# Performance work log

Measured on AMD Instinct MI355X. Metric: run time of the kernel, lower is better.

## Reference

```python
import jax, jax.numpy as jnp
import numpy as np

N, G, S = 51200, 512, 100   # nodes, graphs, nodes per graph
E = 512000                   # edges (within-graph)
F, H, D = 64, 4, 64
HD = H * D                   # 256
C = 10
RATIO = 0.8
NEG = -1e30


def _seg_softmax(logits, seg, mask, num_seg):
    # masked softmax over edges grouped by destination node
    lg = jnp.where(mask[:, None], logits, NEG)
    m = jax.lax.stop_gradient(jax.ops.segment_max(lg, seg, num_segments=num_seg))
    ex = jnp.where(mask[:, None], jnp.exp(lg - m[seg]), 0.0)
    s = jax.ops.segment_sum(ex, seg, num_segments=num_seg)
    return ex / jnp.maximum(s[seg], 1e-16)


def _gat_conv(x, src, dst, nmask, emask, W, att, b, Wres):
    # PyG GATConv: heads=4, concat=True, add_self_loops=True, residual Linear
    h = (x @ W).reshape(N, H, D)
    a_src = (h * att[0]).sum(-1)   # [N,H]
    a_dst = (h * att[1]).sum(-1)
    loop = jnp.arange(N, dtype=src.dtype)
    s2 = jnp.concatenate([src, loop])
    d2 = jnp.concatenate([dst, loop])
    em2 = jnp.concatenate([emask, nmask])
    logits = jax.nn.leaky_relu(a_src[s2] + a_dst[d2], 0.2)   # [E+N,H]
    alpha = _seg_softmax(logits, d2, em2, N)
    out = jax.ops.segment_sum(h[s2] * alpha[:, :, None], d2, num_segments=N)
    out = out.reshape(N, HD) + x @ Wres + b
    return out * nmask[:, None]


def _gt_conv(x, src, dst, nmask, emask, Wqkv, bqkv, Wskip, bskip):
    # PyG TransformerConv: heads=4, concat=True, root_weight=True (lin_skip)
    qkv = (x @ Wqkv + bqkv).reshape(N, 3, H, D)
    q, k, v = qkv[:, 0], qkv[:, 1], qkv[:, 2]
    logits = (q[dst] * k[src]).sum(-1) * (1.0 / np.sqrt(D))   # [E,H]
    alpha = _seg_softmax(logits, dst, emask, N)
    out = jax.ops.segment_sum(v[src] * alpha[:, :, None], dst, num_segments=N)
    return (out.reshape(N, HD) + x @ Wskip + bskip) * nmask[:, None]


def _topk_pool(x, w, batch, nmask, emask, src, dst):
    # PyG TopKPooling: score=tanh(x.w/|w|), keep top ceil(0.8*n) per graph,
    # x <- x*score, drop edges touching removed nodes. Masked (static-shape) form.
    score = jnp.tanh((x @ w) / jnp.linalg.norm(w))
    keyv = jnp.where(nmask, score, NEG)
    # composite key: sort by graph id, then by score descending (dead nodes last)
    ck = batch.astype(jnp.float32) * 4.0 - jnp.clip(keyv, -1.5, 1.5)
    order = jnp.argsort(ck)
    n_alive = jax.ops.segment_sum(nmask.astype(jnp.int32), batch, num_segments=G)
    k = jnp.ceil(RATIO * n_alive.astype(jnp.float32)).astype(jnp.int32)
    counts = jax.ops.segment_sum(jnp.ones(N, jnp.int32), batch, num_segments=G)
    start = jnp.cumsum(counts) - counts
    gs = batch[order]
    rank = jnp.arange(N, dtype=jnp.int32) - start[gs]
    keep = jnp.zeros(N, bool).at[order].set(rank < k[gs]) & nmask
    x_new = jnp.where(keep[:, None], x * score[:, None], 0.0)
    emask_new = emask & keep[src] & keep[dst]
    return x_new, keep, emask_new


def _readout(x, batch, nmask):
    # torch_geometric gmp || gap over alive nodes
    mx = jax.ops.segment_max(jnp.where(nmask[:, None], x, NEG), batch, num_segments=G)
    sm = jax.ops.segment_sum(x * nmask[:, None].astype(x.dtype), batch, num_segments=G)
    cnt = jax.ops.segment_sum(nmask.astype(x.dtype), batch, num_segments=G)
    return jnp.concatenate([mx, sm / jnp.maximum(cnt, 1.0)[:, None]], axis=1)


def _branch(x, src, dst, batch, conv, layers, pool_w):
    nmask = jnp.ones(N, bool)
    emask = jnp.ones(E, bool)
    acc = jnp.zeros((G, 2 * HD), x.dtype)
    for i in range(3):
        x = jax.nn.relu(conv(x, src, dst, nmask, emask, *layers[i]))
        x, nmask, emask = _topk_pool(x, pool_w[i], batch, nmask, emask, src, dst)
        acc = acc + _readout(x, batch, nmask)
    return acc


def _forward(x, edge_index, batch, gat1_W, gat1_att, gat1_b, gat1_res, gat2_W, gat2_att, gat2_b, gat2_res, gat3_W, gat3_att, gat3_b, gat3_res, gat_pool_w, gt1_Wqkv, gt1_bqkv, gt1_Wskip, gt1_bskip, gt2_Wqkv, gt2_bqkv, gt2_Wskip, gt2_bskip, gt3_Wqkv, gt3_bqkv, gt3_Wskip, gt3_bskip, gt_pool_w, lin1_W, lin1_b, lin2_W, lin2_b, lin3_W, lin3_b):
    src, dst = edge_index[0], edge_index[1]
    gat_layers = [(gat1_W, gat1_att, gat1_b, gat1_res),
                  (gat2_W, gat2_att, gat2_b, gat2_res),
                  (gat3_W, gat3_att, gat3_b, gat3_res)]
    gt_layers = [(gt1_Wqkv, gt1_bqkv, gt1_Wskip, gt1_bskip),
                 (gt2_Wqkv, gt2_bqkv, gt2_Wskip, gt2_bskip),
                 (gt3_Wqkv, gt3_bqkv, gt3_Wskip, gt3_bskip)]
    h1 = _branch(x, src, dst, batch, _gat_conv, gat_layers, gat_pool_w)
    h2 = _branch(x, src, dst, batch, _gt_conv, gt_layers, gt_pool_w)
    h = jnp.concatenate([h1, h2], axis=1)   # [G, 1024]
    h = jax.nn.relu(h @ lin1_W + lin1_b)
    # dropout p=0.5 skipped (eval mode)
    h = jax.nn.relu(h @ lin2_W + lin2_b)
    return jax.nn.log_softmax(h @ lin3_W + lin3_b, axis=-1)


def setup_inputs():
    keys = iter(jax.random.split(jax.random.key(0), 64))
    def nrm(shape, scale):
        return jax.random.normal(next(keys), shape, jnp.float32) * scale
    inp = {}
    inp["x"] = nrm((N, F), 1.0)
    src = jax.random.randint(next(keys), (E,), 0, N, jnp.int32)
    off = jax.random.randint(next(keys), (E,), 0, S, jnp.int32)
    dst = (src // S) * S + off   # keep edges within the source node's graph
    inp["edge_index"] = jnp.stack([src, dst])
    inp["batch"] = jnp.arange(N, dtype=jnp.int32) // S
    ins = [F, HD, HD]
    for i in range(3):
        fi = ins[i]
        sc = 1.0 / np.sqrt(fi)
        inp[f"gat{i+1}_W"] = nrm((fi, HD), sc)
        inp[f"gat{i+1}_att"] = nrm((2, H, D), 0.1)
        inp[f"gat{i+1}_b"] = jnp.zeros((HD,), jnp.float32)
        inp[f"gat{i+1}_res"] = nrm((fi, HD), sc)
        inp[f"gt{i+1}_Wqkv"] = nrm((fi, 3 * HD), sc)
        inp[f"gt{i+1}_bqkv"] = jnp.zeros((3 * HD,), jnp.float32)
        inp[f"gt{i+1}_Wskip"] = nrm((fi, HD), sc)
        inp[f"gt{i+1}_bskip"] = jnp.zeros((HD,), jnp.float32)
    inp["gat_pool_w"] = nrm((3, HD), 0.1)
    inp["gt_pool_w"] = nrm((3, HD), 0.1)
    inp["lin1_W"] = nrm((4 * HD, 128), 1.0 / np.sqrt(4 * HD))
    inp["lin1_b"] = jnp.zeros((128,), jnp.float32)
    inp["lin2_W"] = nrm((128, 64), 1.0 / np.sqrt(128.0))
    inp["lin2_b"] = jnp.zeros((64,), jnp.float32)
    inp["lin3_W"] = nrm((64, C), 1.0 / np.sqrt(64.0))
    inp["lin3_b"] = jnp.zeros((C,), jnp.float32)
    return inp


def reference(x, edge_index, batch, gat1_W, gat1_att, gat1_b, gat1_res, gat2_W, gat2_att, gat2_b, gat2_res, gat3_W, gat3_att, gat3_b, gat3_res, gat_pool_w, gt1_Wqkv, gt1_bqkv, gt1_Wskip, gt1_bskip, gt2_Wqkv, gt2_bqkv, gt2_Wskip, gt2_bskip, gt3_Wqkv, gt3_bqkv, gt3_Wskip, gt3_bskip, gt_pool_w, lin1_W, lin1_b, lin2_W, lin2_b, lin3_W, lin3_b):
    return _forward(x, edge_index, batch, gat1_W, gat1_att, gat1_b, gat1_res, gat2_W, gat2_att, gat2_b, gat2_res, gat3_W, gat3_att, gat3_b, gat3_res, gat_pool_w, gt1_Wqkv, gt1_bqkv, gt1_Wskip, gt1_bskip, gt2_Wqkv, gt2_bqkv, gt2_Wskip, gt2_bskip, gt3_Wqkv, gt3_bqkv, gt3_Wskip, gt3_bskip, gt_pool_w, lin1_W, lin1_b, lin2_W, lin2_b, lin3_W, lin3_b)
```

## Files before the change

### kernel.cpp

```cpp
#include <hip/hip_runtime.h>
#include <hip/hip_bf16.h>
#include <math.h>

#define N_NODES 51200
#define N_GRAPHS 512
#define S_NODES 100
#define N_EDGES 512000
#define HDF 256
#define NEGF (-1e30f)
#define DCAP 128

typedef short bf16x8 __attribute__((ext_vector_type(8)));
typedef float f32x4 __attribute__((ext_vector_type(4)));

__device__ inline unsigned short f2b(float x) {
    union { float f; unsigned u; } v; v.f = x;
    unsigned r = v.u + 0x7FFFu + ((v.u >> 16) & 1u);
    return (unsigned short)(r >> 16);
}
__device__ inline float b2f(unsigned short b) {
    union { float f; unsigned u; } v; v.u = ((unsigned)b) << 16; return v.f;
}

__global__ void set_int(int* __restrict__ p, int v, int n) {
    int i = blockIdx.x * 256 + threadIdx.x;
    if (i < n) p[i] = v;
}

__global__ void init_zero(int* __restrict__ deg, int* __restrict__ cursor,
                          float* __restrict__ acc1, float* __restrict__ acc2) {
    int i = blockIdx.x * 256 + threadIdx.x;
    if (i < N_NODES) { deg[i] = 0; cursor[i] = 0; }
    acc1[i] = 0.f;
    acc2[i] = 0.f;
}

struct WSplitDesc { const float* W; unsigned short* Wh; unsigned short* Wl; int K, NC; };
struct WSplitPack { WSplitDesc d[12]; };
__global__ void wsplit_all(WSplitPack p) {
    WSplitDesc d = p.d[blockIdx.y];
    int idx = blockIdx.x * 256 + threadIdx.x;
    if (idx >= d.K * d.NC) return;
    int k = idx / d.NC, c = idx - k * d.NC;
    float v = d.W[idx];
    unsigned short h = f2b(v);
    int o = ((k >> 3) * d.NC + c) * 8 + (k & 7);
    d.Wh[o] = h;
    d.Wl[o] = f2b(v - b2f(h));
}

__global__ __launch_bounds__(512) void mfma_gemm(
    const float* __restrict__ A,
    const unsigned short* __restrict__ Bh_g, const unsigned short* __restrict__ Bl_g,
    const float* __restrict__ bias, float* __restrict__ C,
    int K, int NC,
    const float* __restrict__ agg, int aggStride,
    const int* __restrict__ nmaskArr,
    const float* __restrict__ rowScale, const int* __restrict__ rsMask)
{
    __shared__ unsigned short Ah[4 * 128 * 8];
    __shared__ unsigned short Al[4 * 128 * 8];
    int row0 = blockIdx.y * 128, col0 = blockIdx.x * 256;
    int t = threadIdx.x;
    int lane = t & 63, w = t >> 6;
    int wr = w >> 2, wc = w & 3;
    int l15 = lane & 15, l4 = lane >> 4;
    f32x4 acc[4][4];
    #pragma unroll
    for (int m = 0; m < 4; ++m)
        #pragma unroll
        for (int n = 0; n < 4; ++n) acc[m][n] = (f32x4){0.f, 0.f, 0.f, 0.f};

    int arow = t & 127, akg = t >> 7;
    float ascale = 1.f;
    if (rowScale) ascale = rsMask[row0 + arow] ? rowScale[row0 + arow] : 0.f;

    for (int k0 = 0; k0 < K; k0 += 32) {
        const float* ap = A + (size_t)(row0 + arow) * K + k0 + akg * 8;
        float4 a0 = *(const float4*)ap;
        float4 a1 = *(const float4*)(ap + 4);
        float av[8] = {a0.x, a0.y, a0.z, a0.w, a1.x, a1.y, a1.z, a1.w};
        int abase = (akg * 128 + arow) * 8;
        #pragma unroll
        for (int j = 0; j < 8; ++j) {
            float s = av[j] * ascale;
            unsigned short h = f2b(s);
            Ah[abase + j] = h;
            Al[abase + j] = f2b(s - b2f(h));
        }
        __syncthreads();
        bf16x8 bh[4], bl[4];
        size_t brow = (size_t)((k0 >> 3) + l4) * NC;
        #pragma unroll
        for (int n = 0; n < 4; ++n) {
            size_t gb = (brow + col0 + wc * 64 + n * 16 + l15) * 8;
            bh[n] = *(const bf16x8*)&Bh_g[gb];
            bl[n] = *(const bf16x8*)&Bl_g[gb];
        }
        #pragma unroll
        for (int m = 0; m < 4; ++m) {
            int idx = (l4 * 128 + wr * 64 + m * 16 + l15) * 8;
            bf16x8 ah = *(bf16x8*)&Ah[idx];
            bf16x8 al = *(bf16x8*)&Al[idx];
            #pragma unroll
            for (int n = 0; n < 4; ++n) {
                acc[m][n] = __builtin_amdgcn_mfma_f32_16x16x32_bf16(ah, bh[n], acc[m][n], 0, 0, 0);
                acc[m][n] = __builtin_amdgcn_mfma_f32_16x16x32_bf16(ah, bl[n], acc[m][n], 0, 0, 0);
                acc[m][n] = __builtin_amdgcn_mfma_f32_16x16x32_bf16(al, bh[n], acc[m][n], 0, 0, 0);
            }
        }
        __syncthreads();
    }
    bool fused = (agg != nullptr);
    #pragma unroll
    for (int m = 0; m < 4; ++m) {
        #pragma unroll
        for (int n = 0; n < 4; ++n) {
            int col = col0 + wc * 64 + n * 16 + l15;
            float bv = bias ? bias[col] : 0.f;
            #pragma unroll
            for (int r = 0; r < 4; ++r) {
                int row = row0 + wr * 64 + m * 16 + l4 * 4 + r;
                float v = acc[m][n][r] + bv;
                if (fused) {
                    v += agg[(size_t)row * aggStride + col];
                    float nm = nmaskArr[row] ? 1.f : 0.f;
                    C[(size_t)row * 256 + col] = fmaxf(v, 0.f) * nm;
                } else {
                    C[(size_t)row * NC + col] = v;
                }
            }
        }
    }
}

__global__ void count_deg(const int* __restrict__ dst, int* __restrict__ deg) {
    int e = blockIdx.x * 256 + threadIdx.x;
    atomicAdd(&deg[dst[e]], 1);
}

__global__ __launch_bounds__(1024) void scan_deg(const int* __restrict__ deg,
                                                 int* __restrict__ rowStart) {
    __shared__ int part[1024];
    int t = threadIdx.x;
    const int chunk = N_NODES / 1024;
    int s = t * chunk;
    int sum = 0;
    for (int i = 0; i < chunk; ++i) sum += deg[s + i];
    part[t] = sum;
    __syncthreads();
    for (int d = 1; d < 1024; d <<= 1) {
        int v = (t >= d) ? part[t - d] : 0;
        __syncthreads();
        part[t] += v;
        __syncthreads();
    }
    int excl = (t == 0) ? 0 : part[t - 1];
    for (int i = 0; i < chunk; ++i) { rowStart[s + i] = excl; excl += deg[s + i]; }
    if (t == 1023) rowStart[N_NODES] = part[1023];
}

__global__ void scatter_edges(const int* __restrict__ src, const int* __restrict__ dst,
                              int* __restrict__ cursor, const int* __restrict__ rowStart,
                              int* __restrict__ csrSrc) {
    int e = blockIdx.x * 256 + threadIdx.x;
    int d = dst[e];
    int p = atomicAdd(&cursor[d], 1);
    csrSrc[rowStart[d] + p] = src[e];
}

__global__ __launch_bounds__(256) void gat_att_pw(const float* __restrict__ hfeat,
                                                  const float* __restrict__ att,
                                                  float* __restrict__ aS,
                                                  float* __restrict__ aD) {
    int t = threadIdx.x, w = t >> 6, l = t & 63;
    int i = blockIdx.x * 4 + w;
    int h = l >> 4, g16 = l & 15;
    float4 hv = *(const float4*)&hfeat[i * HDF + l * 4];
    float4 a0 = *(const float4*)&att[l * 4];
    float4 a1 = *(const float4*)&att[256 + l * 4];
    float p0 = hv.x * a0.x + hv.y * a0.y + hv.z * a0.z + hv.w * a0.w;
    float p1 = hv.x * a1.x + hv.y * a1.y + hv.z * a1.z + hv.w * a1.w;
    p0 += __shfl_xor(p0, 1, 64);  p1 += __shfl_xor(p1, 1, 64);
    p0 += __shfl_xor(p0, 2, 64);  p1 += __shfl_xor(p1, 2, 64);
    p0 += __shfl_xor(p0, 4, 64);  p1 += __shfl_xor(p1, 4, 64);
    p0 += __shfl_xor(p0, 8, 64);  p1 += __shfl_xor(p1, 8, 64);
    if (g16 == 0) { aS[i * 4 + h] = p0; aD[i * 4 + h] = p1; }
}

__global__ __launch_bounds__(256) void gat_edge_pg(
    const float* __restrict__ hfeat, const float* __restrict__ aS, const float* __restrict__ aD,
    const int* __restrict__ rowStart, const int* __restrict__ csrSrc,
    const int* __restrict__ nmask,
    float* __restrict__ aggOut)
{
    int bid = blockIdx.x;
    int t = threadIdx.x, w = t >> 6, l = t & 63;
    int i = (bid & 7) * (N_NODES / 8) + (bid >> 3) * 4 + w;
    int h = l >> 4, g16 = l & 15;
    __shared__ float sL[4][4][DCAP + 8];
    __shared__ int   sS[4][DCAP + 8];
    if (!nmask[i]) {
        *(float4*)&aggOut[i * HDF + l * 4] = make_float4(0.f, 0.f, 0.f, 0.f);
        return;
    }
    int rs = rowStart[i];
    int deg = min(rowStart[i + 1] - rs, DCAP);
    float adh = aD[i * 4 + h];
    for (int j = 0; j < deg; ++j) {
        int s_ = csrSrc[rs + j];
        int ok = nmask[s_];
        float lg = aS[s_ * 4 + h] + adh;
        lg = (lg >= 0.f) ? lg : 0.2f * lg;
        if (g16 == 0) sL[w][h][j] = ok ? lg : NEGF;
        if (l == 0) sS[w][j] = ok ? s_ : -1;
    }
    {
        float lg = aS[i * 4 + h] + adh;
        lg = (lg >= 0.f) ? lg : 0.2f * lg;
        if (g16 == 0) sL[w][h][deg] = lg;
        if (l == 0) sS[w][deg] = i;
    }
    int tot = deg + 1;
    float m = NEGF;
    for (int j = g16; j < tot; j += 16) m = fmaxf(m, sL[w][h][j]);
    m = fmaxf(m, __shfl_xor(m, 1, 64));
    m = fmaxf(m, __shfl_xor(m, 2, 64));
    m = fmaxf(m, __shfl_xor(m, 4, 64));
    m = fmaxf(m, __shfl_xor(m, 8, 64));
    float sum = 0.f;
    for (int j = g16; j < tot; j += 16) {
        float lv = sL[w][h][j];
        float e = (lv > -1e29f) ? __expf(lv - m) : 0.f;
        sL[w][h][j] = e;
        sum += e;
    }
    sum += __shfl_xor(sum, 1, 64);
    sum += __shfl_xor(sum, 2, 64);
    sum += __shfl_xor(sum, 4, 64);
    sum += __shfl_xor(sum, 8, 64);
    float inv = 1.f / fmaxf(sum, 1e-16f);
    float4 a4 = make_float4(0.f, 0.f, 0.f, 0.f);
    for (int j = 0; j < tot; ++j) {
        int s_ = sS[w][j];
        if (s_ < 0) continue;
        float a = sL[w][h][j] * inv;
        float4 v4 = *(const float4*)&hfeat[s_ * HDF + l * 4];
        a4.x += a * v4.x; a4.y += a * v4.y; a4.z += a * v4.z; a4.w += a * v4.w;
    }
    *(float4*)&aggOut[i * HDF + l * 4] = a4;
}

__global__ __launch_bounds__(256) void gt_edge_pg(
    float* __restrict__ qkv,
    const int* __restrict__ rowStart, const int* __restrict__ csrSrc,
    const int* __restrict__ nmask)
{
    int bid = blockIdx.x;
    int t = threadIdx.x, w = t >> 6, l = t & 63;
    int i = (bid & 7) * (N_NODES / 8) + (bid >> 3) * 4 + w;
    int h = l >> 4, g16 = l & 15;
    __shared__ float sL[4][4][DCAP + 8];
    __shared__ int   sS[4][DCAP + 8];
    if (!nmask[i]) {
        *(float4*)&qkv[i * 768 + l * 4] = make_float4(0.f, 0.f, 0.f, 0.f);
        return;
    }
    int rs = rowStart[i];
    int deg = min(rowStart[i + 1] - rs, DCAP);
    float4 q4 = *(const float4*)&qkv[i * 768 + l * 4];
    for (int j = 0; j < deg; ++j) {
        int s_ = csrSrc[rs + j];
        int ok = nmask[s_];
        float4 k4 = *(const float4*)&qkv[s_ * 768 + 256 + l * 4];
        float p = q4.x * k4.x + q4.y * k4.y + q4.z * k4.z + q4.w * k4.w;
        p += __shfl_xor(p, 1, 64);
        p += __shfl_xor(p, 2, 64);
        p += __shfl_xor(p, 4, 64);
        p += __shfl_xor(p, 8, 64);
        if (g16 == 0) sL[w][h][j] = ok ? p * 0.125f : NEGF;
        if (l == 0) sS[w][j] = ok ? s_ : -1;
    }
    float m = NEGF;
    for (int j = g16; j < deg; j += 16) m = fmaxf(m, sL[w][h][j]);
    m = fmaxf(m, __shfl_xor(m, 1, 64));
    m = fmaxf(m, __shfl_xor(m, 2, 64));
    m = fmaxf(m, __shfl_xor(m, 4, 64));
    m = fmaxf(m, __shfl_xor(m, 8, 64));
    float sum = 0.f;
    for (int j = g16; j < deg; j += 16) {
        float lv = sL[w][h][j];
        float e = (lv > -1e29f) ? __expf(lv - m) : 0.f;
        sL[w][h][j] = e;
        sum += e;
    }
    sum += __shfl_xor(sum, 1, 64);
    sum += __shfl_xor(sum, 2, 64);
    sum += __shfl_xor(sum, 4, 64);
    sum += __shfl_xor(sum, 8, 64);
    float inv = 1.f / fmaxf(sum, 1e-16f);
    float4 a4 = make_float4(0.f, 0.f, 0.f, 0.f);
    for (int j = 0; j < deg; ++j) {
        int s_ = sS[w][j];
        if (s_ < 0) continue;
        float a = sL[w][h][j] * inv;
        float4 v4 = *(const float4*)&qkv[s_ * 768 + 512 + l * 4];
        a4.x += a * v4.x; a4.y += a * v4.y; a4.z += a * v4.z; a4.w += a * v4.w;
    }
    *(float4*)&qkv[i * 768 + l * 4] = a4;
}

__global__ __launch_bounds__(256) void spr_kernel(
    const float* __restrict__ x, const float* __restrict__ w,
    float* __restrict__ score, int* __restrict__ nmask, float* __restrict__ acc)
{
    int g = blockIdx.x, t = threadIdx.x;
    int wv = t >> 6, l = t & 63;
    __shared__ float sW[256];
    __shared__ float sRaw[104];
    __shared__ float sFin[104];
    __shared__ int   sKeep[104];
    __shared__ float swn;
    __shared__ int cnt_s;
    if (t == 0) cnt_s = 0;
    sW[t] = w[t];
    __syncthreads();
    if (wv == 0) {
        float dw = 0.f;
        #pragma unroll
        for (int c = 0; c < 4; ++c) { float v = sW[l + c * 64]; dw += v * v; }
        #pragma unroll
        for (int o = 32; o > 0; o >>= 1) dw += __shfl_down(dw, o, 64);
        if (l == 0) swn = sqrtf(dw);
    }
    int base = g * S_NODES;
    for (int u = 0; u < 25; ++u) {
        int nl = wv * 25 + u;
        float dx = 0.f;
        #pragma unroll
        for (int c = 0; c < 4; ++c) {
            int cc = l + c * 64;
            dx += x[(size_t)(base + nl) * HDF + cc] * sW[cc];
        }
        #pragma unroll
        for (int o = 32; o > 0; o >>= 1) dx += __shfl_down(dx, o, 64);
        if (l == 0) sRaw[nl] = dx;
    }
    __syncthreads();
    int alive = 0;
    float ck = -2.0f;
    if (t < S_NODES) {
        float sc = tanhf(sRaw[t] / swn);
        sFin[t] = sc;
        score[base + t] = sc;
        alive = nmask[base + t];
        ck = alive ? sc : -1.5f;
        sRaw[t] = ck;
        if (alive) atomicAdd(&cnt_s, 1);
    }
    __syncthreads();
    int k = (int)ceilf(0.8f * (float)cnt_s);
    if (t < S_NODES) {
        int rank = 0;
        for (int jj = 0; jj < S_NODES; ++jj) {
            float o = sRaw[jj];
            rank += (o > ck || (o == ck && jj < t)) ? 1 : 0;
        }
        int kp = (alive && rank < k) ? 1 : 0;
        sKeep[t] = kp;
        nmask[base + t] = kp;
    }
    __syncthreads();
    float mx = NEGF, sm = 0.f, cnt = 0.f;
    for (int o = 0; o < S_NODES; o += 4) {
        float v0 = x[(size_t)(base + o + 0) * HDF + t];
        float v1 = x[(size_t)(base + o + 1) * HDF + t];
        float v2 = x[(size_t)(base + o + 2) * HDF + t];
        float v3 = x[(size_t)(base + o + 3) * HDF + t];
        if (sKeep[o + 0]) { float v = v0 * sFin[o + 0]; mx = fmaxf(mx, v); sm += v; cnt += 1.f; }
        if (sKeep[o + 1]) { float v = v1 * sFin[o + 1]; mx = fmaxf(mx, v); sm += v; cnt += 1.f; }
        if (sKeep[o + 2]) { float v = v2 * sFin[o + 2]; mx = fmaxf(mx, v); sm += v; cnt += 1.f; }
        if (sKeep[o + 3]) { float v = v3 * sFin[o + 3]; mx = fmaxf(mx, v); sm += v; cnt += 1.f; }
    }
    acc[(size_t)g * 512 + t] += mx;
    acc[(size_t)g * 512 + 256 + t] += sm / fmaxf(cnt, 1.f);
}

__global__ __launch_bounds__(128) void mlp_kernel(
    const float* __restrict__ acc1, const float* __restrict__ acc2,
    const float* __restrict__ W1, const float* __restrict__ b1,
    const float* __restrict__ W2, const float* __restrict__ b2,
    const float* __restrict__ W3, const float* __restrict__ b3,
    float* __restrict__ out)
{
    int g = blockIdx.x, t = threadIdx.x;
    __shared__ float hrow[1024];
    __shared__ float h1s[128];
    __shared__ float h2s[64];
    __shared__ float o3[10];
    for (int j = t; j < 512; j += 128) {
        hrow[j] = acc1[(size_t)g * 512 + j];
        hrow[512 + j] = acc2[(size_t)g * 512 + j];
    }
    __syncthreads();
    float s = b1[t];
    for (int kx = 0; kx < 1024; ++kx) s += hrow[kx] * W1[(size_t)kx * 128 + t];
    h1s[t] = fmaxf(s, 0.f);
    __syncthreads();
    if (t < 64) {
        float s2 = b2[t];
        for (int kx = 0; kx < 128; ++kx) s2 += h1s[kx] * W2[kx * 64 + t];
        h2s[t] = fmaxf(s2, 0.f);
    }
    __syncthreads();
    if (t < 10) {
        float s3 = b3[t];
        for (int kx = 0; kx < 64; ++kx) s3 += h2s[kx] * W3[kx * 10 + t];
        o3[t] = s3;
    }
    __syncthreads();
    if (t < 10) {
        float m = o3[0];
        for (int j = 1; j < 10; ++j) m = fmaxf(m, o3[j]);
        float se = 0.f;
        for (int j = 0; j < 10; ++j) se += expf(o3[j] - m);
        out[g * 10 + t] = o3[t] - m - logf(se);
    }
}

extern "C" void kernel_launch(void* const* d_in, const int* in_sizes, int n_in,
                              void* d_out, int out_size, void* d_ws, size_t ws_size,
                              hipStream_t stream) {
    (void)n_in; (void)out_size; (void)ws_size;
    const float* x0 = (const float*)d_in[0];
    const int* src = (const int*)d_in[1];
    const int* dst = src + N_EDGES;

    bool dictOrder = (in_sizes[7] == 64 * 768);
    const float *gatW[3], *gatAtt[3], *gatB[3], *gatRes[3];
    const float *gtWqkv[3], *gtBqkv[3], *gtWskip[3], *gtBskip[3];
    const float *gatPool, *gtPool;
    if (dictOrder) {
        for (int l = 0; l < 3; ++l) {
            int b = 3 + l * 8;
            gatW[l]    = (const float*)d_in[b + 0];
            gatAtt[l]  = (const float*)d_in[b + 1];
            gatB[l]    = (const float*)d_in[b + 2];
            gatRes[l]  = (const float*)d_in[b + 3];
            gtWqkv[l]  = (const float*)d_in[b + 4];
            gtBqkv[l]  = (const float*)d_in[b + 5];
            gtWskip[l] = (const float*)d_in[b + 6];
            gtBskip[l] = (const float*)d_in[b + 7];
        }
        gatPool = (const float*)d_in[27];
        gtPool  = (const float*)d_in[28];
    } else {
        for (int l = 0; l < 3; ++l) {
            int b = 3 + l * 4;
            gatW[l]   = (const float*)d_in[b + 0];
            gatAtt[l] = (const float*)d_in[b + 1];
            gatB[l]   = (const float*)d_in[b + 2];
            gatRes[l] = (const float*)d_in[b + 3];
            int c = 16 + l * 4;
            gtWqkv[l]  = (const float*)d_in[c + 0];
            gtBqkv[l]  = (const float*)d_in[c + 1];
            gtWskip[l] = (const float*)d_in[c + 2];
            gtBskip[l] = (const float*)d_in[c + 3];
        }
        gatPool = (const float*)d_in[15];
        gtPool  = (const float*)d_in[28];
    }
    const float* lin1W = (const float*)d_in[29];
    const float* lin1b = (const float*)d_in[30];
    const float* lin2W = (const float*)d_in[31];
    const float* lin2b = (const float*)d_in[32];
    const float* lin3W = (const float*)d_in[33];
    const float* lin3b = (const float*)d_in[34];

    char* wsp = (char*)d_ws;
    size_t off = 0;
    auto carve = [&](size_t bytes) -> void* {
        void* p = wsp + off;
        off += (bytes + 255) & ~(size_t)255;
        return p;
    };
    float* bufX   = (float*)carve((size_t)N_NODES * HDF * 4);
    float* bufH   = (float*)carve((size_t)N_NODES * 768 * 4);
    float* aS     = (float*)carve((size_t)N_NODES * 4 * 4);
    float* aD     = (float*)carve((size_t)N_NODES * 4 * 4);
    float* scoreB = (float*)carve((size_t)N_NODES * 4);
    int* nmask    = (int*)carve((size_t)N_NODES * 4);
    int* deg      = (int*)carve((size_t)N_NODES * 4);
    int* rowStart = (int*)carve((size_t)(N_NODES + 1) * 4);
    int* cursor   = (int*)carve((size_t)N_NODES * 4);
    int* csrSrc   = (int*)carve((size_t)N_EDGES * 4);
    float* acc1   = (float*)carve((size_t)N_GRAPHS * 512 * 4);
    float* acc2   = (float*)carve((size_t)N_GRAPHS * 512 * 4);
    const int wElems = 884736;
    unsigned short* whBase = (unsigned short*)carve((size_t)wElems * 2);
    unsigned short* wlBase = (unsigned short*)carve((size_t)wElems * 2);
    float* ysec   = bufH + (size_t)N_NODES * HDF;

    unsigned short *WH[12], *WL[12];
    {
        WSplitPack pack;
        int o = 0, maxSz = 0;
        for (int l = 0; l < 3; ++l) {
            int fi = (l == 0) ? 64 : 256;
            int sz[4] = {fi * 256, fi * 256, fi * 768, fi * 256};
            const float* Wp[4] = {gatW[l], gatRes[l], gtWqkv[l], gtWskip[l]};
            int NCs[4] = {256, 256, 768, 256};
            for (int q = 0; q < 4; ++q) {
                int idx = l * 4 + q;
                WH[idx] = whBase + o;
                WL[idx] = wlBase + o;
                pack.d[idx] = {Wp[q], WH[idx], WL[idx], fi, NCs[q]};
                if (sz[q] > maxSz) maxSz = sz[q];
                o += sz[q];
            }
        }
        wsplit_all<<<dim3((maxSz + 255) / 256, 12), 256, 0, stream>>>(pack);
    }

    init_zero<<<(N_GRAPHS * 512) / 256, 256, 0, stream>>>(deg, cursor, acc1, acc2);
    count_deg<<<N_EDGES / 256, 256, 0, stream>>>(dst, deg);
    scan_deg<<<1, 1024, 0, stream>>>(deg, rowStart);
    scatter_edges<<<N_EDGES / 256, 256, 0, stream>>>(src, dst, cursor, rowStart, csrSrc);

    for (int br = 0; br < 2; ++br) {
        bool isGAT = (br == 0);
        float* acc = isGAT ? acc1 : acc2;
        const float* poolW = isGAT ? gatPool : gtPool;
        set_int<<<N_NODES / 256, 256, 0, stream>>>(nmask, 1, N_NODES);
        const float* xcur = x0;
        int fi = 64;
        for (int l = 0; l < 3; ++l) {
            const float* rs = (l == 0) ? nullptr : scoreB;
            const int* rsm = (l == 0) ? nullptr : nmask;
            if (isGAT) {
                mfma_gemm<<<dim3(1, N_NODES / 128), 512, 0, stream>>>(
                    xcur, WH[l * 4 + 0], WL[l * 4 + 0], nullptr, bufH, fi, 256,
                    nullptr, 0, nullptr, rs, rsm);
                gat_att_pw<<<N_NODES / 4, 256, 0, stream>>>(bufH, gatAtt[l], aS, aD);
                gat_edge_pg<<<N_NODES / 4, 256, 0, stream>>>(bufH, aS, aD, rowStart,
                                                             csrSrc, nmask, ysec);
                mfma_gemm<<<dim3(1, N_NODES / 128), 512, 0, stream>>>(
                    xcur, WH[l * 4 + 1], WL[l * 4 + 1], gatB[l], bufX, fi, 256,
                    ysec, HDF, nmask, rs, rsm);
            } else {
                mfma_gemm<<<dim3(3, N_NODES / 128), 512, 0, stream>>>(
                    xcur, WH[l * 4 + 2], WL[l * 4 + 2], gtBqkv[l], bufH, fi, 768,
                    nullptr, 0, nullptr, rs, rsm);
                gt_edge_pg<<<N_NODES / 4, 256, 0, stream>>>(bufH, rowStart, csrSrc,
                                                            nmask);
                mfma_gemm<<<dim3(1, N_NODES / 128), 512, 0, stream>>>(
                    xcur, WH[l * 4 + 3], WL[l * 4 + 3], gtBskip[l], bufX, fi, 256,
                    bufH , 768, nmask, rs, rsm);
            }
            spr_kernel<<<N_GRAPHS, 256, 0, stream>>>(bufX, poolW + l * HDF,
                                                     scoreB, nmask, acc);
            xcur = bufX;
            fi = HDF;
        }
    }
    mlp_kernel<<<N_GRAPHS, 128, 0, stream>>>(acc1, acc2, lin1W, lin1b, lin2W, lin2b,
                                             lin3W, lin3b, (float*)d_out);
}
```

Baseline: 1.329 ms.

## Double-buffer GEMM A tiles and parallelize edge neighbor preload in GAT/GT kernels

The MFMA GEMM now uses two LDS buffers for the A tile. It prefetches the next K-slice from global memory while the current slice is consumed, which drops one barrier per iteration. The GAT and GT edge kernels load neighbor indices and masks in parallel across the wavefront into shared memory, replacing a serial per-edge loop. GAT logits are also computed in parallel across the 16 lanes per head, and GT skips K loads for masked neighbors. The cost is double the LDS use in the GEMM, which may lower occupancy.

```diff
diff --git a/kernel.cpp b/kernel.cpp
--- a/kernel.cpp
+++ b/kernel.cpp
@@ -58,8 +58,8 @@
     const int* __restrict__ nmaskArr,
     const float* __restrict__ rowScale, const int* __restrict__ rsMask)
 {
-    __shared__ unsigned short Ah[4 * 128 * 8];
-    __shared__ unsigned short Al[4 * 128 * 8];
+    __shared__ unsigned short Ah[2][4 * 128 * 8];
+    __shared__ unsigned short Al[2][4 * 128 * 8];
     int row0 = blockIdx.y * 128, col0 = blockIdx.x * 256;
     int t = threadIdx.x;
     int lane = t & 63, w = t >> 6;
@@ -74,21 +74,31 @@
     int arow = t & 127, akg = t >> 7;
     float ascale = 1.f;
     if (rowScale) ascale = rsMask[row0 + arow] ? rowScale[row0 + arow] : 0.f;
-
-    for (int k0 = 0; k0 < K; k0 += 32) {
-        const float* ap = A + (size_t)(row0 + arow) * K + k0 + akg * 8;
-        float4 a0 = *(const float4*)ap;
-        float4 a1 = *(const float4*)(ap + 4);
+    const float* aptr = A + (size_t)(row0 + arow) * K + akg * 8;
+    int abase = (akg * 128 + arow) * 8;
+
+    {
+        float4 a0 = *(const float4*)aptr;
+        float4 a1 = *(const float4*)(aptr + 4);
         float av[8] = {a0.x, a0.y, a0.z, a0.w, a1.x, a1.y, a1.z, a1.w};
-        int abase = (akg * 128 + arow) * 8;
         #pragma unroll
         for (int j = 0; j < 8; ++j) {
             float s = av[j] * ascale;
             unsigned short h = f2b(s);
-            Ah[abase + j] = h;
-            Al[abase + j] = f2b(s - b2f(h));
-        }
-        __syncthreads();
+            Ah[0][abase + j] = h;
+            Al[0][abase + j] = f2b(s - b2f(h));
+        }
+    }
+    __syncthreads();
+
+    for (int k0 = 0; k0 < K; k0 += 32) {
+        int cur = (k0 >> 5) & 1;
+        bool more = (k0 + 32) < K;
+        float4 n0, n1;
+        if (more) {
+            n0 = *(const float4*)(aptr + k0 + 32);
+            n1 = *(const float4*)(aptr + k0 + 36);
+        }
         bf16x8 bh[4], bl[4];
         size_t brow = (size_t)((k0 >> 3) + l4) * NC;
         #pragma unroll
@@ -100,13 +110,23 @@
         #pragma unroll
         for (int m = 0; m < 4; ++m) {
             int idx = (l4 * 128 + wr * 64 + m * 16 + l15) * 8;
-            bf16x8 ah = *(bf16x8*)&Ah[idx];
-            bf16x8 al = *(bf16x8*)&Al[idx];
+            bf16x8 ah = *(bf16x8*)&Ah[cur][idx];
+            bf16x8 al = *(bf16x8*)&Al[cur][idx];
             #pragma unroll
             for (int n = 0; n < 4; ++n) {
                 acc[m][n] = __builtin_amdgcn_mfma_f32_16x16x32_bf16(ah, bh[n], acc[m][n], 0, 0, 0);
                 acc[m][n] = __builtin_amdgcn_mfma_f32_16x16x32_bf16(ah, bl[n], acc[m][n], 0, 0, 0);
                 acc[m][n] = __builtin_amdgcn_mfma_f32_16x16x32_bf16(al, bh[n], acc[m][n], 0, 0, 0);
+            }
+        }
+        if (more) {
+            float nv[8] = {n0.x, n0.y, n0.z, n0.w, n1.x, n1.y, n1.z, n1.w};
+            #pragma unroll
+            for (int j = 0; j < 8; ++j) {
+                float s = nv[j] * ascale;
+                unsigned short h = f2b(s);
+                Ah[cur ^ 1][abase + j] = h;
+                Al[cur ^ 1][abase + j] = f2b(s - b2f(h));
             }
         }
         __syncthreads();
@@ -206,20 +226,24 @@
     }
     int rs = rowStart[i];
     int deg = min(rowStart[i + 1] - rs, DCAP);
+    for (int j = l; j < deg; j += 64) {
+        int s_ = csrSrc[rs + j];
+        sS[w][j] = nmask[s_] ? s_ : -1;
+    }
+    if (l == 0) sS[w][deg] = i;
     float adh = aD[i * 4 + h];
-    for (int j = 0; j < deg; ++j) {
-        int s_ = csrSrc[rs + j];
-        int ok = nmask[s_];
-        float lg = aS[s_ * 4 + h] + adh;
-        lg = (lg >= 0.f) ? lg : 0.2f * lg;
-        if (g16 == 0) sL[w][h][j] = ok ? lg : NEGF;
-        if (l == 0) sS[w][j] = ok ? s_ : -1;
-    }
-    {
+    for (int j = g16; j < deg; j += 16) {
+        int s_ = sS[w][j];
+        float lg = NEGF;
+        if (s_ >= 0) {
+            lg = aS[s_ * 4 + h] + adh;
+            lg = (lg >= 0.f) ? lg : 0.2f * lg;
+        }
+        sL[w][h][j] = lg;
+    }
+    if (g16 == (deg & 15)) {
         float lg = aS[i * 4 + h] + adh;
-        lg = (lg >= 0.f) ? lg : 0.2f * lg;
-        if (g16 == 0) sL[w][h][deg] = lg;
-        if (l == 0) sS[w][deg] = i;
+        sL[w][h][deg] = (lg >= 0.f) ? lg : 0.2f * lg;
     }
     int tot = deg + 1;
     float m = NEGF;
@@ -268,18 +292,23 @@
     }
     int rs = rowStart[i];
     int deg = min(rowStart[i + 1] - rs, DCAP);
+    for (int j = l; j < deg; j += 64) {
+        int s_ = csrSrc[rs + j];
+        sS[w][j] = nmask[s_] ? s_ : -1;
+    }
     float4 q4 = *(const float4*)&qkv[i * 768 + l * 4];
     for (int j = 0; j < deg; ++j) {
-        int s_ = csrSrc[rs + j];
-        int ok = nmask[s_];
-        float4 k4 = *(const float4*)&qkv[s_ * 768 + 256 + l * 4];
-        float p = q4.x * k4.x + q4.y * k4.y + q4.z * k4.z + q4.w * k4.w;
+        int s_ = sS[w][j];
+        float p = 0.f;
+        if (s_ >= 0) {
+            float4 k4 = *(const float4*)&qkv[s_ * 768 + 256 + l * 4];
+            p = q4.x * k4.x + q4.y * k4.y + q4.z * k4.z + q4.w * k4.w;
+        }
         p += __shfl_xor(p, 1, 64);
         p += __shfl_xor(p, 2, 64);
         p += __shfl_xor(p, 4, 64);
         p += __shfl_xor(p, 8, 64);
-        if (g16 == 0) sL[w][h][j] = ok ? p * 0.125f : NEGF;
-        if (l == 0) sS[w][j] = ok ? s_ : -1;
+        if (g16 == 0) sL[w][h][j] = (s_ >= 0) ? p * 0.125f : NEGF;
     }
     float m = NEGF;
     for (int j = g16; j < deg; j += 16) m = fmaxf(m, sL[w][h][j]);
```

Result: slower. 1.423 ms (+7.1%).
